# Performance work log

Hardware: AMD Instinct MI355X
Metric: run time of the kernel (lower is better)

Reference implementation:

```python
import jax, jax.numpy as jnp
import numpy as np

B, N, DIM = 2, 2048, 1024
H, KVH, DH = 16, 4, 64
SCALE = DH ** -0.5


def setup_inputs() -> dict:
    key = jax.random.key(0)
    ks = jax.random.split(key, 7)
    x = jax.random.normal(ks[0], (B, N, DIM), dtype=jnp.float32)
    mask = jax.random.randint(ks[1], (N, N), 0, 2).astype(jnp.bool_)
    Wq = jax.random.normal(ks[2], (DIM, H * DH), dtype=jnp.float32) * (DIM ** -0.5)
    Wk = jax.random.normal(ks[3], (DIM, KVH * DH), dtype=jnp.float32) * (DIM ** -0.5)
    Wv = jax.random.normal(ks[4], (DIM, KVH * DH), dtype=jnp.float32) * (DIM ** -0.5)
    Wo = jax.random.normal(ks[5], (H * DH, DIM), dtype=jnp.float32) * ((H * DH) ** -0.5)
    bo = jnp.zeros((DIM,), dtype=jnp.float32)
    return {"x": x, "mask": mask, "Wq": Wq, "Wk": Wk, "Wv": Wv, "Wo": Wo, "bo": bo}


def reference(x, mask, Wq, Wk, Wv, Wo, bo):
    b, n, _ = x.shape
    # projections -> [b, h, n, dh]
    q = (x @ Wq).reshape(b, n, H, DH).transpose(0, 2, 1, 3)
    k = (x @ Wk).reshape(b, n, KVH, DH).transpose(0, 2, 1, 3)
    v = (x @ Wv).reshape(b, n, KVH, DH).transpose(0, 2, 1, 3)
    # GQA: repeat kv heads, 'b h n d -> b (h r) n d'
    r = H // KVH
    k = jnp.repeat(k, r, axis=1)
    v = jnp.repeat(v, r, axis=1)
    dots = jnp.einsum('bhnd,bhmd->bhnm', q, k) * SCALE  # [b,h,n,n]
    dots = jnp.where(mask, jnp.float32(-1e9), dots)
    attn = jax.nn.softmax(dots, axis=-1)  # dropout p=0.0 -> identity
    out = jnp.einsum('bhnm,bhmd->bhnd', attn, v)
    out = out.transpose(0, 2, 1, 3).reshape(b, n, H * DH)
    return out @ Wo + bo
```

## Files before the change

kernel.cpp:

```cpp
#include <hip/hip_runtime.h>
#include <stdint.h>

typedef unsigned short u16;
typedef u16 u16x8 __attribute__((ext_vector_type(8)));
typedef u16 u16x4 __attribute__((ext_vector_type(4)));
typedef float f32x4 __attribute__((ext_vector_type(4)));

#define AS1(p) ((const __attribute__((address_space(1))) void*)(p))
#define AS3(p) ((__attribute__((address_space(3))) void*)(p))

__device__ __forceinline__ void gload16(void* lds, const void* g) {
  __builtin_amdgcn_global_load_lds(AS1(g), AS3(lds), 16, 0, 0);
}

__device__ __forceinline__ u16 f2bf(float f) {
  union { float f; uint32_t u; } c; c.f = f;
  uint32_t u = c.u + 0x7FFFu + ((c.u >> 16) & 1u);
  return (u16)(u >> 16);
}

__device__ __forceinline__ void mfma16(f32x4& d, u16x8 a, u16x8 b) {
  asm("v_mfma_f32_16x16x32_bf16 %0, %1, %2, %0" : "+v"(d) : "v"(a), "v"(b));
}

__global__ void prep(const float* __restrict__ x, u16* __restrict__ xb,
                     const void* __restrict__ mraw, unsigned long long* __restrict__ mb,
                     const float* __restrict__ Wq, const float* __restrict__ Wk,
                     const float* __restrict__ Wv, const float* __restrict__ Wo,
                     u16* __restrict__ Wcat, u16* __restrict__ WoT) {
  __shared__ float t[64][65];
  const int bi = blockIdx.x, tid = threadIdx.x;
  if (bi < 4096) {
    int i = (bi * 256 + tid) * 4;
    float4 v = *(const float4*)(x + i);
    u16x4 o; o.x = f2bf(v.x); o.y = f2bf(v.y); o.z = f2bf(v.z); o.w = f2bf(v.w);
    *(u16x4*)(xb + i) = o;
  } else if (bi < 20480) {
    const int lane = tid & 63;
    const uint32_t* mi = (const uint32_t*)mraw;
    const bool int_mode = __all(mi[lane] <= 1u);
    const int wid = ((bi - 4096) * 256 + tid) >> 6;
    const size_t base = (size_t)(wid >> 5) * 2048 + (size_t)(wid & 31) * 64 + lane;
    bool bit;
    if (int_mode) bit = mi[base] != 0;
    else          bit = ((const uint8_t*)mraw)[base] != 0;
    unsigned long long bm = __ballot(bit);
    if (lane == 0) mb[wid] = bm;
  } else {
    const float* in; u16* out; int R, C, bx, by, lb;
    if (bi < 20736)      { lb = bi - 20480; in = Wq; out = Wcat;              R = 1024; C = 1024; bx = lb & 15; by = lb >> 4; }
    else if (bi < 20800) { lb = bi - 20736; in = Wk; out = Wcat + 1024*1024;  R = 1024; C = 256;  bx = lb & 3;  by = lb >> 2; }
    else if (bi < 20864) { lb = bi - 20800; in = Wv; out = Wcat + 1280*1024;  R = 1024; C = 256;  bx = lb & 3;  by = lb >> 2; }
    else                 { lb = bi - 20864; in = Wo; out = WoT;               R = 1024; C = 1024; bx = lb & 15; by = lb >> 4; }
    const int c0 = bx * 64, r0 = by * 64;
#pragma unroll
    for (int k = 0; k < 4; ++k) {
      int idx = k * 256 + tid;
      int r = idx >> 4, c = (idx & 15) * 4;
      float4 v = *(const float4*)(in + (size_t)(r0 + r) * C + c0 + c);
      t[r][c] = v.x; t[r][c + 1] = v.y; t[r][c + 2] = v.z; t[r][c + 3] = v.w;
    }
    __syncthreads();
#pragma unroll
    for (int k = 0; k < 4; ++k) {
      int idx = k * 256 + tid;
      int c = idx >> 4, r = (idx & 15) * 4;
      u16x4 o;
      o.x = f2bf(t[r][c]); o.y = f2bf(t[r + 1][c]);
      o.z = f2bf(t[r + 2][c]); o.w = f2bf(t[r + 3][c]);
      *(u16x4*)(out + (size_t)(c0 + c) * R + r0 + r) = o;
    }
  }
}

#define SCALE_LOG2 0.18033688011112042f

template <int EPI, int BM, int BN>
__global__ __launch_bounds__(256, 4) void gemm_bt(
    const u16* __restrict__ A, const u16* __restrict__ Bt,
    u16* __restrict__ Qb, u16* __restrict__ Kb, u16* __restrict__ VTb,
    float* __restrict__ Co, const float* __restrict__ bias) {
  constexpr int MR = BM / 32, NR = BN / 32;
  __shared__ u16 As[BM * 32];
  __shared__ u16 Bs[BN * 32];
  const int tid = threadIdx.x, lane = tid & 63, wave = tid >> 6;
  const int wr = wave >> 1, wc = wave & 1;
  const int lg = lane >> 4, ll = lane & 15;
  const int bm = blockIdx.x * BM, bn = blockIdx.y * BN;
  const int K = 1024;
  const u16* Ag = A + (size_t)bm * K;
  const u16* Bg = Bt + (size_t)bn * K;

  f32x4 acc[MR][NR];
#pragma unroll
  for (int m = 0; m < MR; ++m)
#pragma unroll
    for (int n = 0; n < NR; ++n) acc[m][n] = f32x4{0.f, 0.f, 0.f, 0.f};

  const int r0 = tid >> 2, c0 = (tid & 3) * 8;

  for (int k0 = 0; k0 < K; k0 += 32) {
    gload16(&As[(size_t)tid * 8], Ag + (size_t)r0 * K + k0 + c0);
    if constexpr (BM == 128)
      gload16(&As[(size_t)(256 + tid) * 8], Ag + (size_t)(64 + r0) * K + k0 + c0);
    gload16(&Bs[(size_t)tid * 8], Bg + (size_t)r0 * K + k0 + c0);
    if constexpr (BN == 128)
      gload16(&Bs[(size_t)(256 + tid) * 8], Bg + (size_t)(64 + r0) * K + k0 + c0);
    __syncthreads();
    u16x8 af[MR], bf[NR];
#pragma unroll
    for (int m = 0; m < MR; ++m) af[m] = *(const u16x8*)&As[(wr * (BM/2) + m * 16 + ll) * 32 + lg * 8];
#pragma unroll
    for (int n = 0; n < NR; ++n) bf[n] = *(const u16x8*)&Bs[(wc * (BN/2) + n * 16 + ll) * 32 + lg * 8];
#pragma unroll
    for (int m = 0; m < MR; ++m)
#pragma unroll
      for (int n = 0; n < NR; ++n) mfma16(acc[m][n], af[m], bf[n]);
    __syncthreads();
  }

  const int row0 = bm + wr * (BM/2) + lg * 4;
  const int col0 = bn + wc * (BN/2) + ll;
#pragma unroll
  for (int m = 0; m < MR; ++m) {
#pragma unroll
    for (int n = 0; n < NR; ++n) {
      const int col = col0 + n * 16;
#pragma unroll
      for (int r = 0; r < 4; ++r) {
        const int row = row0 + m * 16 + r;
        const float v = acc[m][n][r];
        if (EPI == 0) {
          const int b = row >> 11, t = row & 2047;
          if (col < 1024) {
            Qb[((size_t)(b * 16 + (col >> 6)) * 2048 + t) * 64 + (col & 63)] = f2bf(v * SCALE_LOG2);
          } else if (col < 1280) {
            const int c2 = col - 1024;
            Kb[((size_t)(b * 4 + (c2 >> 6)) * 2048 + t) * 64 + (c2 & 63)] = f2bf(v);
          } else {
            const int c2 = col - 1280;
            VTb[((size_t)(b * 4 + (c2 >> 6)) * 64 + (c2 & 63)) * 2048 + t] = f2bf(v);
          }
        } else {
          Co[(size_t)row * 1024 + col] = v + bias[col];
        }
      }
    }
  }
}


__device__ __forceinline__ void stage_kv(u16* Kl, u16* Vl,
                                         const u16* Kg, const u16* Vg,
                                         int kv0, int tid) {
  const int i0 = tid, i1 = 256 + tid;
  const int ra = i0 >> 3, sa = (i0 & 7) ^ (ra & 7);
  const int rb = i1 >> 3, sb = (i1 & 7) ^ (rb & 7);
  gload16(&Kl[(size_t)i0 * 8], Kg + (size_t)(kv0 + ra) * 64 + sa * 8);
  gload16(&Kl[(size_t)i1 * 8], Kg + (size_t)(kv0 + rb) * 64 + sb * 8);
  gload16(&Vl[(size_t)i0 * 8], Vg + (size_t)ra * 2048 + kv0 + sa * 8);
  gload16(&Vl[(size_t)i1 * 8], Vg + (size_t)rb * 2048 + kv0 + sb * 8);
}

__global__ __launch_bounds__(256, 2) void attn(
    const u16* __restrict__ Qb, const u16* __restrict__ Kb, const u16* __restrict__ VTb,
    const unsigned long long* __restrict__ mb, u16* __restrict__ Ob) {
  __shared__ u16 Klds[2][64 * 64];
  __shared__ u16 Vlds[2][64 * 64];
  __shared__ u16 Plds[4][32 * 64];
  const int tid = threadIdx.x, lane = tid & 63, wave = tid >> 6;
  const int lg = lane >> 4, ll = lane & 15;
  const int qt = blockIdx.x, h = blockIdx.y, b = blockIdx.z;
  const int kvh = h >> 2;
  const u16* Qg = Qb + ((size_t)(b * 16 + h) * 2048 + qt * 128 + wave * 32) * 64;
  const u16* Kg = Kb + (size_t)(b * 4 + kvh) * 2048 * 64;
  const u16* Vg = VTb + (size_t)(b * 4 + kvh) * 64 * 2048;
  u16* Pw = Plds[wave];
  const int sw = (ll & 7) << 3;

  u16x8 qf[2][2];
#pragma unroll
  for (int qb2 = 0; qb2 < 2; ++qb2)
#pragma unroll
    for (int kc = 0; kc < 2; ++kc)
      qf[qb2][kc] = *(const u16x8*)&Qg[(qb2 * 16 + ll) * 64 + kc * 32 + lg * 8];

  f32x4 o[2][4];
#pragma unroll
  for (int qb2 = 0; qb2 < 2; ++qb2)
#pragma unroll
    for (int db = 0; db < 4; ++db) o[qb2][db] = f32x4{0.f, 0.f, 0.f, 0.f};
  float mx[2] = {-3e9f, -3e9f}, ls[2] = {0.f, 0.f};
  const int qrow0 = qt * 128 + wave * 32;

  stage_kv(Klds[0], Vlds[0], Kg, Vg, 0, tid);

  for (int c = 0; c < 32; ++c) {
    const int cur = c & 1;
    const u16* Kl = Klds[cur];
    const u16* Vl = Vlds[cur];
    const unsigned long long w0 = mb[(size_t)(qrow0 + ll) * 32 + c];
    const unsigned long long w1 = mb[(size_t)(qrow0 + 16 + ll) * 32 + c];
    if (c < 31) {
      stage_kv(Klds[cur ^ 1], Vlds[cur ^ 1], Kg, Vg, (c + 1) * 64, tid);
      asm volatile("s_waitcnt vmcnt(4)" ::: "memory");
    } else {
      asm volatile("s_waitcnt vmcnt(0)" ::: "memory");
    }
    __builtin_amdgcn_s_barrier();
    asm volatile("" ::: "memory");

    f32x4 sf[2][4];
#pragma unroll
    for (int qb2 = 0; qb2 < 2; ++qb2)
#pragma unroll
      for (int kt = 0; kt < 4; ++kt) sf[qb2][kt] = f32x4{0.f, 0.f, 0.f, 0.f};
#pragma unroll
    for (int kt = 0; kt < 4; ++kt) {
      const int krow = kt * 16 + ll;
#pragma unroll
      for (int kc = 0; kc < 2; ++kc) {
        u16x8 kf = *(const u16x8*)&Kl[(krow * 64 + kc * 32 + lg * 8) ^ ((krow & 7) << 3)];
        mfma16(sf[0][kt], kf, qf[0][kc]);
        mfma16(sf[1][kt], kf, qf[1][kc]);
      }
    }

    float p[2][4][4], smax[2];
#pragma unroll
    for (int qb2 = 0; qb2 < 2; ++qb2) {
      const unsigned long long w = qb2 ? w1 : w0;
      float m0 = -3e9f;
#pragma unroll
      for (int kt = 0; kt < 4; ++kt)
#pragma unroll
        for (int r = 0; r < 4; ++r) {
          float s = sf[qb2][kt][r];
          s = ((w >> (kt * 16 + lg * 4 + r)) & 1ull) ? -3e9f : s;
          p[qb2][kt][r] = s;
          m0 = fmaxf(m0, s);
        }
      m0 = fmaxf(m0, __shfl_xor(m0, 16));
      m0 = fmaxf(m0, __shfl_xor(m0, 32));
      smax[qb2] = m0;
    }

    const bool upd = (smax[0] > mx[0] + 8.f) || (smax[1] > mx[1] + 8.f);
    if (__any(upd)) {
      float av[2];
#pragma unroll
      for (int qb2 = 0; qb2 < 2; ++qb2) {
        const float mn = fmaxf(mx[qb2], smax[qb2]);
        av[qb2] = exp2f(mx[qb2] - mn);
        mx[qb2] = mn;
        ls[qb2] *= av[qb2];
      }
#pragma unroll
      for (int r = 0; r < 4; ++r) {
        const float a0 = __shfl(av[0], lg * 4 + r);
        const float a1 = __shfl(av[1], lg * 4 + r);
#pragma unroll
        for (int db = 0; db < 4; ++db) { o[0][db][r] *= a0; o[1][db][r] *= a1; }
      }
    }

#pragma unroll
    for (int qb2 = 0; qb2 < 2; ++qb2) {
      const int q = qb2 * 16 + ll;
      float psum = 0.f;
#pragma unroll
      for (int kt = 0; kt < 4; ++kt) {
        float e0 = exp2f(p[qb2][kt][0] - mx[qb2]);
        float e1 = exp2f(p[qb2][kt][1] - mx[qb2]);
        float e2 = exp2f(p[qb2][kt][2] - mx[qb2]);
        float e3 = exp2f(p[qb2][kt][3] - mx[qb2]);
        psum += (e0 + e1) + (e2 + e3);
        u16x4 pk; pk.x = f2bf(e0); pk.y = f2bf(e1); pk.z = f2bf(e2); pk.w = f2bf(e3);
        *(u16x4*)&Pw[q * 64 + ((kt * 16 + lg * 4) ^ sw)] = pk;
      }
      psum += __shfl_xor(psum, 16);
      psum += __shfl_xor(psum, 32);
      ls[qb2] += psum;
    }

    asm volatile("" ::: "memory");
    __builtin_amdgcn_sched_barrier(0);

#pragma unroll
    for (int kc = 0; kc < 2; ++kc) {
      u16x8 pf[2];
#pragma unroll
      for (int qb2 = 0; qb2 < 2; ++qb2) {
        const int q = qb2 * 16 + ll;
        pf[qb2] = *(const u16x8*)&Pw[q * 64 + ((kc * 32 + lg * 8) ^ sw)];
      }
#pragma unroll
      for (int db = 0; db < 4; ++db) {
        const int d = db * 16 + ll;
        u16x8 vf = *(const u16x8*)&Vl[(d * 64 + kc * 32 + lg * 8) ^ ((d & 7) << 3)];
        mfma16(o[0][db], pf[0], vf);
        mfma16(o[1][db], pf[1], vf);
      }
    }
    asm volatile("s_waitcnt lgkmcnt(0)" ::: "memory");
    __builtin_amdgcn_s_barrier();
    asm volatile("" ::: "memory");
  }

#pragma unroll
  for (int qb2 = 0; qb2 < 2; ++qb2) {
#pragma unroll
    for (int r = 0; r < 4; ++r) {
      const float lsr = __shfl(ls[qb2], lg * 4 + r);
      const float inv = 1.f / lsr;
      const int tok = qt * 128 + wave * 32 + qb2 * 16 + lg * 4 + r;
#pragma unroll
      for (int db = 0; db < 4; ++db)
        Ob[(size_t)(b * 2048 + tok) * 1024 + h * 64 + db * 16 + ll] = f2bf(o[qb2][db][r] * inv);
    }
  }
}

extern "C" void kernel_launch(void* const* d_in, const int* in_sizes, int n_in,
                              void* d_out, int out_size, void* d_ws, size_t ws_size,
                              hipStream_t stream) {
  const float* x  = (const float*)d_in[0];
  const void*  mk = d_in[1];
  const float* Wq = (const float*)d_in[2];
  const float* Wk = (const float*)d_in[3];
  const float* Wv = (const float*)d_in[4];
  const float* Wo = (const float*)d_in[5];
  const float* bo = (const float*)d_in[6];
  float* out = (float*)d_out;

  char* ws = (char*)d_ws;
  size_t off = 0;
  auto alloc = [&](size_t bytes) { void* p = ws + off; off += (bytes + 255) & ~(size_t)255; return p; };
  u16* xb   = (u16*)alloc(4096ull * 1024 * 2);
  u16* Wcat = (u16*)alloc(1536ull * 1024 * 2);
  u16* WoT  = (u16*)alloc(1024ull * 1024 * 2);
  u16* Qb   = (u16*)alloc(2ull * 16 * 2048 * 64 * 2);
  u16* Kb   = (u16*)alloc(2ull * 4 * 2048 * 64 * 2);
  u16* VTb  = (u16*)alloc(2ull * 4 * 64 * 2048 * 2);
  u16* Ob   = (u16*)alloc(4096ull * 1024 * 2);
  unsigned long long* mbits = (unsigned long long*)alloc(65536ull * 8);
  (void)ws_size; (void)in_sizes; (void)n_in; (void)out_size;

  prep<<<21120, 256, 0, stream>>>(x, xb, mk, mbits, Wq, Wk, Wv, Wo, Wcat, WoT);
  gemm_bt<0, 64, 128><<<dim3(64, 12), 256, 0, stream>>>(xb, Wcat, Qb, Kb, VTb, nullptr, nullptr);
  attn<<<dim3(16, 16, 2), 256, 0, stream>>>(Qb, Kb, VTb, mbits, Ob);
  gemm_bt<1, 128, 64><<<dim3(32, 16), 256, 0, stream>>>(Ob, WoT, nullptr, nullptr, nullptr, out, bo);
}
```

Before: 157.2 us.

## Double GEMM K-tile to 64 with XOR-swizzled LDS layout

The bf16 GEMM now stages a K-slice of 64 instead of 32 per iteration, which halves the number of barrier pairs per output tile. It also stores LDS rows with an XOR swizzle on the 16-byte chunk index to avoid bank conflicts when reading fragments. LDS use per block doubles, which may reduce occupancy under the launch bound of 4 blocks per CU.

```diff
diff --git a/kernel.cpp b/kernel.cpp
--- a/kernel.cpp
+++ b/kernel.cpp
@@ -81,8 +81,8 @@
     u16* __restrict__ Qb, u16* __restrict__ Kb, u16* __restrict__ VTb,
     float* __restrict__ Co, const float* __restrict__ bias) {
   constexpr int MR = BM / 32, NR = BN / 32;
-  __shared__ u16 As[BM * 32];
-  __shared__ u16 Bs[BN * 32];
+  __shared__ u16 As[BM * 64];
+  __shared__ u16 Bs[BN * 64];
   const int tid = threadIdx.x, lane = tid & 63, wave = tid >> 6;
   const int wr = wave >> 1, wc = wave & 1;
   const int lg = lane >> 4, ll = lane & 15;
@@ -97,30 +97,45 @@
 #pragma unroll
     for (int n = 0; n < NR; ++n) acc[m][n] = f32x4{0.f, 0.f, 0.f, 0.f};
 
-  const int r0 = tid >> 2, c0 = (tid & 3) * 8;
-
-  for (int k0 = 0; k0 < K; k0 += 32) {
-    gload16(&As[(size_t)tid * 8], Ag + (size_t)r0 * K + k0 + c0);
-    if constexpr (BM == 128)
-      gload16(&As[(size_t)(256 + tid) * 8], Ag + (size_t)(64 + r0) * K + k0 + c0);
-    gload16(&Bs[(size_t)tid * 8], Bg + (size_t)r0 * K + k0 + c0);
-    if constexpr (BN == 128)
-      gload16(&Bs[(size_t)(256 + tid) * 8], Bg + (size_t)(64 + r0) * K + k0 + c0);
+  for (int k0 = 0; k0 < K; k0 += 64) {
+#pragma unroll
+    for (int i = 0; i < MR; ++i) {
+      const int idx = i * 256 + tid;
+      const int row = idx >> 3;
+      const int s = (idx & 7) ^ (row & 7);
+      gload16(&As[(size_t)idx * 8], Ag + (size_t)row * K + k0 + s * 8);
+    }
+#pragma unroll
+    for (int i = 0; i < NR; ++i) {
+      const int idx = i * 256 + tid;
+      const int row = idx >> 3;
+      const int s = (idx & 7) ^ (row & 7);
+      gload16(&Bs[(size_t)idx * 8], Bg + (size_t)row * K + k0 + s * 8);
+    }
     __syncthreads();
-    u16x8 af[MR], bf[NR];
-#pragma unroll
-    for (int m = 0; m < MR; ++m) af[m] = *(const u16x8*)&As[(wr * (BM/2) + m * 16 + ll) * 32 + lg * 8];
-#pragma unroll
-    for (int n = 0; n < NR; ++n) bf[n] = *(const u16x8*)&Bs[(wc * (BN/2) + n * 16 + ll) * 32 + lg * 8];
-#pragma unroll
-    for (int m = 0; m < MR; ++m)
-#pragma unroll
-      for (int n = 0; n < NR; ++n) mfma16(acc[m][n], af[m], bf[n]);
+#pragma unroll
+    for (int kk = 0; kk < 2; ++kk) {
+      u16x8 af[MR], bf[NR];
+#pragma unroll
+      for (int m = 0; m < MR; ++m) {
+        const int row = wr * (BM / 2) + m * 16 + ll;
+        af[m] = *(const u16x8*)&As[(row * 64 + kk * 32 + lg * 8) ^ ((row & 7) << 3)];
+      }
+#pragma unroll
+      for (int n = 0; n < NR; ++n) {
+        const int row = wc * (BN / 2) + n * 16 + ll;
+        bf[n] = *(const u16x8*)&Bs[(row * 64 + kk * 32 + lg * 8) ^ ((row & 7) << 3)];
+      }
+#pragma unroll
+      for (int m = 0; m < MR; ++m)
+#pragma unroll
+        for (int n = 0; n < NR; ++n) mfma16(acc[m][n], af[m], bf[n]);
+    }
     __syncthreads();
   }
 
-  const int row0 = bm + wr * (BM/2) + lg * 4;
-  const int col0 = bn + wc * (BN/2) + ll;
+  const int row0 = bm + wr * (BM / 2) + lg * 4;
+  const int col0 = bn + wc * (BN / 2) + ll;
 #pragma unroll
   for (int m = 0; m < MR; ++m) {
 #pragma unroll
```

Result: faster. 148.3 us (-5.7%).
